# Performance work log

Hardware: AMD Instinct MI355X
Metric: run time of the kernel (lower is better)

## Reference

```python
import jax, jax.numpy as jnp
import numpy as np

BETA = 0.1
EPS_LOW = 0.2
EPS_HIGH = 0.2
TEMPERATURE = 1.0


def setup_inputs() -> dict:
    key = jax.random.key(0)
    ks = jax.random.split(key, 6)
    B, T, H, V = 4, 1024, 2048, 32000
    x = jax.random.normal(ks[0], (B, T, H), dtype=jnp.float32)
    ref_input = jax.random.normal(ks[1], (B, T, H), dtype=jnp.float32)
    W = jax.random.normal(ks[2], (V, H), dtype=jnp.float32) * (1.0 / np.sqrt(H))
    ref_W = jax.random.normal(ks[3], (V, H), dtype=jnp.float32) * (1.0 / np.sqrt(H))
    selected_token_ids = jax.random.randint(ks[4], (B, T), 0, V, dtype=jnp.int64)
    attention_mask = jnp.ones((B, T), dtype=jnp.float32)
    advantages = jax.random.normal(ks[5], (B,), dtype=jnp.float32)
    return {
        "x": x,
        "W": W,
        "ref_W": ref_W,
        "ref_input": ref_input,
        "selected_token_ids": selected_token_ids,
        "attention_mask": attention_mask,
        "advantages": advantages,
    }


def _per_token_logps_and_mean(h, W, ids):
    # h: [B,T,H], W: [V,H] -> logits [B,T,V]
    logits = jnp.einsum("bth,vh->btv", h, W)
    if TEMPERATURE != 1.0:
        logits = logits / TEMPERATURE
    log_probs = jax.nn.log_softmax(logits, axis=-1)
    ptl = jnp.take_along_axis(log_probs, ids[..., None], axis=-1)[..., 0]
    return ptl, log_probs.mean()


def reference(x, W, ref_W, ref_input, selected_token_ids, attention_mask, advantages):
    per_token_logps, log_probs_mean = _per_token_logps_and_mean(x, W, selected_token_ids)

    # reference model path (no grad)
    ref_per_token_logps, _ = _per_token_logps_and_mean(
        jax.lax.stop_gradient(ref_input), jax.lax.stop_gradient(ref_W), selected_token_ids
    )
    ref_per_token_logps = jax.lax.stop_gradient(ref_per_token_logps)

    old_per_token_logps = jax.lax.stop_gradient(per_token_logps)
    coef_1 = jnp.exp(per_token_logps - old_per_token_logps)
    coef_2 = jnp.clip(coef_1, 1.0 - EPS_LOW, 1.0 + EPS_HIGH)
    adv = advantages[:, None]  # [B,1]
    per_token_loss = -jnp.minimum(coef_1 * adv, coef_2 * adv)

    delta = ref_per_token_logps - per_token_logps
    kl_div = jnp.exp(delta) - delta - 1.0
    per_token_loss = per_token_loss + BETA * kl_div

    loss = (per_token_loss * attention_mask).sum() / jnp.clip(attention_mask.sum(), 1.0)

    kl_metric = ((kl_div * attention_mask).sum(axis=1) / jnp.clip(attention_mask.sum(axis=1), 1.0)).mean()
    return loss, per_token_logps.mean(), log_probs_mean, kl_metric
```

## Files before the change

### kernel.cpp

```cpp
#include <hip/hip_runtime.h>
#include <stdint.h>

#define M_TOK 4096
#define N_VOC 32000
#define K_DIM 2048
#define BM 128
#define BN 128
#define BK 64
#define BETA 0.1f
#define W_SCALE 32.0f
#define INV_W_SCALE (1.0f / 32.0f)

typedef float f32x4 __attribute__((ext_vector_type(4)));

__global__ __launch_bounds__(256) void cast_f32_fp8(const float* __restrict__ in,
                                                    uint2* __restrict__ out, int n8,
                                                    float scale) {
  int i = blockIdx.x * blockDim.x + threadIdx.x;
  int stride = gridDim.x * blockDim.x;
  const float4* in4 = (const float4*)in;
  for (; i < n8; i += stride) {
    float4 f0 = in4[2 * i];
    float4 f1 = in4[2 * i + 1];
    int lo = __builtin_amdgcn_cvt_pk_fp8_f32(f0.x * scale, f0.y * scale, 0, false);
    lo = __builtin_amdgcn_cvt_pk_fp8_f32(f0.z * scale, f0.w * scale, lo, true);
    int hi = __builtin_amdgcn_cvt_pk_fp8_f32(f1.x * scale, f1.y * scale, 0, false);
    hi = __builtin_amdgcn_cvt_pk_fp8_f32(f1.z * scale, f1.w * scale, hi, true);
    uint2 o;
    o.x = (unsigned)lo;
    o.y = (unsigned)hi;
    out[i] = o;
  }
}

__global__ __launch_bounds__(256) void gemm_stats(
    const unsigned char* __restrict__ A,
    const unsigned char* __restrict__ B,
    const int* __restrict__ ids,
    float* __restrict__ S, float* __restrict__ L, float* __restrict__ sel) {
  __shared__ unsigned char lA[BM * BK];
  __shared__ unsigned char lB[BN * BK];

  const int tid = threadIdx.x;
  const int wid = tid >> 6;
  const int lane = tid & 63;
  const int m0 = blockIdx.y * BM;
  const int n0 = blockIdx.x * BN;
  const int wr = wid >> 1, wc = wid & 1;
  const int l15 = lane & 15, quad = lane >> 4;

  const int sRow = lane >> 2;
  const int sChunk = (lane & 3) ^ ((sRow >> 1) & 3);
  const int sCol = sChunk * 16;

  f32x4 acc[4][4];
  const f32x4 zero = {0.f, 0.f, 0.f, 0.f};
#pragma unroll
  for (int i = 0; i < 4; ++i)
#pragma unroll
    for (int j = 0; j < 4; ++j) acc[i][j] = zero;

  const int swzkey = (l15 >> 1) & 3;

  for (int k0 = 0; k0 < K_DIM; k0 += BK) {
#pragma unroll
    for (int q = 0; q < 2; ++q) {
      int seg = wid * 2 + q;
      int row = seg * 16 + sRow;
      const unsigned char* ga = A + (size_t)(m0 + row) * K_DIM + k0 + sCol;
      const unsigned char* gb = B + (size_t)(n0 + row) * K_DIM + k0 + sCol;
      __builtin_amdgcn_global_load_lds(
          (const __attribute__((address_space(1))) unsigned int*)ga,
          (__attribute__((address_space(3))) unsigned int*)(&lA[seg * 1024]), 16, 0, 0);
      __builtin_amdgcn_global_load_lds(
          (const __attribute__((address_space(1))) unsigned int*)gb,
          (__attribute__((address_space(3))) unsigned int*)(&lB[seg * 1024]), 16, 0, 0);
    }
    __syncthreads();
#pragma unroll
    for (int ks = 0; ks < 2; ++ks) {
      long long af[4], bfr[4];
      const int cg = ks * 2 + (quad >> 1);
      const int coff = ((cg ^ swzkey) * 16) + (quad & 1) * 8;
#pragma unroll
      for (int i = 0; i < 4; ++i) {
        int r = wr * 64 + i * 16 + l15;
        af[i] = *(const long long*)&lA[r * BK + coff];
      }
#pragma unroll
      for (int j = 0; j < 4; ++j) {
        int r = wc * 64 + j * 16 + l15;
        bfr[j] = *(const long long*)&lB[r * BK + coff];
      }
#pragma unroll
      for (int i = 0; i < 4; ++i)
#pragma unroll
        for (int j = 0; j < 4; ++j)
          acc[i][j] = __builtin_amdgcn_mfma_f32_16x16x32_fp8_fp8(af[i], bfr[j], acc[i][j], 0, 0, 0);
    }
    __syncthreads();
  }

#pragma unroll
  for (int i = 0; i < 4; ++i) {
#pragma unroll
    for (int r = 0; r < 4; ++r) {
      int row = m0 + wr * 64 + i * 16 + quad * 4 + r;
      int sid = ids[row];
      int loc = sid - n0 - wc * 64;
      bool hit = (loc >= 0) && (loc < 64) && ((loc & 15) == l15);
      float es = 0.f, ls = 0.f, selv = 0.f;
#pragma unroll
      for (int j = 0; j < 4; ++j) {
        float v = acc[i][j][r] * INV_W_SCALE;
        es += __expf(v);
        ls += v;
        if (hit && ((loc >> 4) == j)) selv = v;
      }
      if (hit) sel[row] = selv;
#pragma unroll
      for (int mk = 1; mk < 16; mk <<= 1) {
        es += __shfl_xor(es, mk);
        ls += __shfl_xor(ls, mk);
      }
      if (l15 == 0) {
        atomicAdd(&S[row], es);
        atomicAdd(&L[row], ls);
      }
    }
  }
}

__global__ __launch_bounds__(1024) void finalize_kernel(
    const float* __restrict__ S1, const float* __restrict__ L1, const float* __restrict__ P1,
    const float* __restrict__ S2, const float* __restrict__ P2,
    const float* __restrict__ mask, const float* __restrict__ adv, float* __restrict__ out) {
  __shared__ float red[12];
  int tid = threadIdx.x;
  int lane = tid & 63;
  if (tid < 12) red[tid] = 0.f;
  __syncthreads();

  float loss_num = 0.f, mask_sum = 0.f, ptl_sum = 0.f, lpm_sum = 0.f;
  float klb[4] = {0.f, 0.f, 0.f, 0.f}, mb[4] = {0.f, 0.f, 0.f, 0.f};
#pragma unroll
  for (int k = 0; k < 4; ++k) {
    int t = k * 1024 + tid;
    float lse1 = logf(S1[t]);
    float ptl = P1[t] - lse1;
    float ref_ptl = P2[t] - logf(S2[t]);
    float d = ref_ptl - ptl;
    float kl = expf(d) - d - 1.f;
    float m = mask[t];
    float a = adv[k];
    loss_num += (-a + BETA * kl) * m;
    mask_sum += m;
    ptl_sum += ptl;
    lpm_sum += L1[t] * (1.f / (float)N_VOC) - lse1;
    klb[k] += kl * m;
    mb[k] += m;
  }
  float vals[12] = {loss_num, mask_sum, ptl_sum, lpm_sum,
                    klb[0], klb[1], klb[2], klb[3],
                    mb[0],  mb[1],  mb[2],  mb[3]};
#pragma unroll
  for (int v = 0; v < 12; ++v) {
    float xv = vals[v];
#pragma unroll
    for (int mk = 32; mk >= 1; mk >>= 1) xv += __shfl_xor(xv, mk);
    if (lane == 0) atomicAdd(&red[v], xv);
  }
  __syncthreads();
  if (tid == 0) {
    float loss = red[0] / fmaxf(red[1], 1.f);
    float km = 0.f;
#pragma unroll
    for (int b = 0; b < 4; ++b) km += red[4 + b] / fmaxf(red[8 + b], 1.f);
    out[0] = loss;
    out[1] = red[2] * (1.f / 4096.f);
    out[2] = red[3] * (1.f / 4096.f);
    out[3] = km * 0.25f;
  }
}

extern "C" void kernel_launch(void* const* d_in, const int* in_sizes, int n_in,
                              void* d_out, int out_size, void* d_ws, size_t ws_size,
                              hipStream_t stream) {
  const float* x = (const float*)d_in[0];
  const float* W = (const float*)d_in[1];
  const float* ref_W = (const float*)d_in[2];
  const float* ref_x = (const float*)d_in[3];
  const int* ids = (const int*)d_in[4];
  const float* mask = (const float*)d_in[5];
  const float* adv = (const float*)d_in[6];
  float* out = (float*)d_out;

  char* ws = (char*)d_ws;
  unsigned char* Wq = (unsigned char*)ws;
  unsigned char* xq = (unsigned char*)(ws + (size_t)N_VOC * K_DIM);
  float* accum = (float*)(ws + (size_t)N_VOC * K_DIM + (size_t)M_TOK * K_DIM);
  float* S1 = accum;
  float* L1 = accum + 4096;
  float* P1 = accum + 8192;
  float* S2 = accum + 12288;
  float* L2 = accum + 16384;
  float* P2 = accum + 20480;

  hipMemsetAsync(accum, 0, 6 * 4096 * sizeof(float), stream);

  dim3 grid(N_VOC / BN, M_TOK / BM);

  cast_f32_fp8<<<2048, 256, 0, stream>>>(W, (uint2*)Wq, N_VOC * K_DIM / 8, W_SCALE);
  cast_f32_fp8<<<512, 256, 0, stream>>>(x, (uint2*)xq, M_TOK * K_DIM / 8, 1.0f);
  gemm_stats<<<grid, 256, 0, stream>>>(xq, Wq, ids, S1, L1, P1);

  cast_f32_fp8<<<2048, 256, 0, stream>>>(ref_W, (uint2*)Wq, N_VOC * K_DIM / 8, W_SCALE);
  cast_f32_fp8<<<512, 256, 0, stream>>>(ref_x, (uint2*)xq, M_TOK * K_DIM / 8, 1.0f);
  gemm_stats<<<grid, 256, 0, stream>>>(xq, Wq, ids, S2, L2, P2);

  finalize_kernel<<<1, 1024, 0, stream>>>(S1, L1, P1, S2, P2, mask, adv, out);
}
```

Measured before the change: 1.976 ms.

## Switch fp8 GEMM to 16x16x128 scaled MFMA with BK=128 and new LDS swizzle

Replaces the 16x16x32 fp8 MFMA with the gfx950 16x16x128 f8f6f4 scaled MFMA using unit scales. The K tile doubles to 128, LDS staging becomes 8 rows by 128 bytes per segment with an XOR swizzle, and each lane loads 32 bytes per operand. The aim is to cut MFMA issue count and K-loop iterations (and the barriers that go with them) in the two big logit GEMMs. The cast kernel is also changed to handle 4 floats per iteration. LDS use doubles and the layout must exactly match the MFMA operand ordering, so correctness depends on the fragment mapping.

```diff
diff --git a/kernel.cpp b/kernel.cpp
--- a/kernel.cpp
+++ b/kernel.cpp
@@ -6,30 +6,26 @@
 #define K_DIM 2048
 #define BM 128
 #define BN 128
-#define BK 64
+#define BK 128
 #define BETA 0.1f
 #define W_SCALE 32.0f
 #define INV_W_SCALE (1.0f / 32.0f)
 
 typedef float f32x4 __attribute__((ext_vector_type(4)));
+typedef int i32x4 __attribute__((ext_vector_type(4)));
+typedef int i32x8 __attribute__((ext_vector_type(8)));
 
 __global__ __launch_bounds__(256) void cast_f32_fp8(const float* __restrict__ in,
-                                                    uint2* __restrict__ out, int n8,
+                                                    unsigned* __restrict__ out, int n4,
                                                     float scale) {
   int i = blockIdx.x * blockDim.x + threadIdx.x;
   int stride = gridDim.x * blockDim.x;
-  const float4* in4 = (const float4*)in;
-  for (; i < n8; i += stride) {
-    float4 f0 = in4[2 * i];
-    float4 f1 = in4[2 * i + 1];
-    int lo = __builtin_amdgcn_cvt_pk_fp8_f32(f0.x * scale, f0.y * scale, 0, false);
-    lo = __builtin_amdgcn_cvt_pk_fp8_f32(f0.z * scale, f0.w * scale, lo, true);
-    int hi = __builtin_amdgcn_cvt_pk_fp8_f32(f1.x * scale, f1.y * scale, 0, false);
-    hi = __builtin_amdgcn_cvt_pk_fp8_f32(f1.z * scale, f1.w * scale, hi, true);
-    uint2 o;
-    o.x = (unsigned)lo;
-    o.y = (unsigned)hi;
-    out[i] = o;
+  const float4* __restrict__ in4 = (const float4*)in;
+  for (; i < n4; i += stride) {
+    float4 f = in4[i];
+    int v = __builtin_amdgcn_cvt_pk_fp8_f32(f.x * scale, f.y * scale, 0, false);
+    v = __builtin_amdgcn_cvt_pk_fp8_f32(f.z * scale, f.w * scale, v, true);
+    out[i] = (unsigned)v;
   }
 }
 
@@ -49,9 +45,12 @@
   const int wr = wid >> 1, wc = wid & 1;
   const int l15 = lane & 15, quad = lane >> 4;
 
-  const int sRow = lane >> 2;
-  const int sChunk = (lane & 3) ^ ((sRow >> 1) & 3);
-  const int sCol = sChunk * 16;
+  const int sRow = lane >> 3;
+  const int sCol = (((lane & 7) ^ sRow) << 4);
+
+  const int swz = l15 & 7;
+  const int cOff0 = (((2 * quad) ^ swz) << 4);
+  const int cOff1 = (((2 * quad + 1) ^ swz) << 4);
 
   f32x4 acc[4][4];
   const f32x4 zero = {0.f, 0.f, 0.f, 0.f};
@@ -60,13 +59,11 @@
 #pragma unroll
     for (int j = 0; j < 4; ++j) acc[i][j] = zero;
 
-  const int swzkey = (l15 >> 1) & 3;
-
   for (int k0 = 0; k0 < K_DIM; k0 += BK) {
 #pragma unroll
-    for (int q = 0; q < 2; ++q) {
-      int seg = wid * 2 + q;
-      int row = seg * 16 + sRow;
+    for (int q = 0; q < 4; ++q) {
+      int seg = wid * 4 + q;
+      int row = seg * 8 + sRow;
       const unsigned char* ga = A + (size_t)(m0 + row) * K_DIM + k0 + sCol;
       const unsigned char* gb = B + (size_t)(n0 + row) * K_DIM + k0 + sCol;
       __builtin_amdgcn_global_load_lds(
@@ -77,26 +74,25 @@
           (__attribute__((address_space(3))) unsigned int*)(&lB[seg * 1024]), 16, 0, 0);
     }
     __syncthreads();
-#pragma unroll
-    for (int ks = 0; ks < 2; ++ks) {
-      long long af[4], bfr[4];
-      const int cg = ks * 2 + (quad >> 1);
-      const int coff = ((cg ^ swzkey) * 16) + (quad & 1) * 8;
-#pragma unroll
-      for (int i = 0; i < 4; ++i) {
-        int r = wr * 64 + i * 16 + l15;
-        af[i] = *(const long long*)&lA[r * BK + coff];
-      }
-#pragma unroll
-      for (int j = 0; j < 4; ++j) {
-        int r = wc * 64 + j * 16 + l15;
-        bfr[j] = *(const long long*)&lB[r * BK + coff];
-      }
+
+    i32x8 af[4];
+#pragma unroll
+    for (int i = 0; i < 4; ++i) {
+      const unsigned char* base = &lA[(wr * 64 + i * 16 + l15) * BK];
+      i32x4 lo = *(const i32x4*)(base + cOff0);
+      i32x4 hi = *(const i32x4*)(base + cOff1);
+      af[i] = __builtin_shufflevector(lo, hi, 0, 1, 2, 3, 4, 5, 6, 7);
+    }
+#pragma unroll
+    for (int j = 0; j < 4; ++j) {
+      const unsigned char* base = &lB[(wc * 64 + j * 16 + l15) * BK];
+      i32x4 lo = *(const i32x4*)(base + cOff0);
+      i32x4 hi = *(const i32x4*)(base + cOff1);
+      i32x8 bf = __builtin_shufflevector(lo, hi, 0, 1, 2, 3, 4, 5, 6, 7);
 #pragma unroll
       for (int i = 0; i < 4; ++i)
-#pragma unroll
-        for (int j = 0; j < 4; ++j)
-          acc[i][j] = __builtin_amdgcn_mfma_f32_16x16x32_fp8_fp8(af[i], bfr[j], acc[i][j], 0, 0, 0);
+        acc[i][j] = __builtin_amdgcn_mfma_scale_f32_16x16x128_f8f6f4(
+            af[i], bf, acc[i][j], 0, 0, 0, 0x7F7F7F7F, 0, 0x7F7F7F7F);
     }
     __syncthreads();
   }
@@ -210,12 +206,12 @@
 
   dim3 grid(N_VOC / BN, M_TOK / BM);
 
-  cast_f32_fp8<<<2048, 256, 0, stream>>>(W, (uint2*)Wq, N_VOC * K_DIM / 8, W_SCALE);
-  cast_f32_fp8<<<512, 256, 0, stream>>>(x, (uint2*)xq, M_TOK * K_DIM / 8, 1.0f);
+  cast_f32_fp8<<<2048, 256, 0, stream>>>(W, (unsigned*)Wq, N_VOC * K_DIM / 4, W_SCALE);
+  cast_f32_fp8<<<512, 256, 0, stream>>>(x, (unsigned*)xq, M_TOK * K_DIM / 4, 1.0f);
   gemm_stats<<<grid, 256, 0, stream>>>(xq, Wq, ids, S1, L1, P1);
 
-  cast_f32_fp8<<<2048, 256, 0, stream>>>(ref_W, (uint2*)Wq, N_VOC * K_DIM / 8, W_SCALE);
-  cast_f32_fp8<<<512, 256, 0, stream>>>(ref_x, (uint2*)xq, M_TOK * K_DIM / 8, 1.0f);
+  cast_f32_fp8<<<2048, 256, 0, stream>>>(ref_W, (unsigned*)Wq, N_VOC * K_DIM / 4, W_SCALE);
+  cast_f32_fp8<<<512, 256, 0, stream>>>(ref_x, (unsigned*)xq, M_TOK * K_DIM / 4, 1.0f);
   gemm_stats<<<grid, 256, 0, stream>>>(xq, Wq, ids, S2, L2, P2);
 
   finalize_kernel<<<1, 1024, 0, stream>>>(S1, L1, P1, S2, P2, mask, adv, out);
```

Result: slower. 4.160 ms (+110.6%).
